# Performance work log

Measured on AMD Instinct MI355X. Metric: run time of the kernel, lower is better.

Reference implementation:

```python
import jax, jax.numpy as jnp
import numpy as np

EMBED, HEADS, WIN = 512, 1, 16  # head_dim == EMBED since HEADS == 1
B, S = 4, 2048


def setup_inputs() -> dict:
    key = jax.random.key(0)
    ks = jax.random.split(key, 9)
    sc = 1.0 / np.sqrt(EMBED)
    return {
        "x": jax.random.normal(ks[0], (B, S, EMBED), dtype=jnp.float32),
        "Wq": jax.random.normal(ks[1], (EMBED, EMBED), dtype=jnp.float32) * sc,
        "bq": jax.random.normal(ks[2], (EMBED,), dtype=jnp.float32) * 0.01,
        "Wk": jax.random.normal(ks[3], (EMBED, EMBED), dtype=jnp.float32) * sc,
        "bk": jax.random.normal(ks[4], (EMBED,), dtype=jnp.float32) * 0.01,
        "Wv": jax.random.normal(ks[5], (EMBED, EMBED), dtype=jnp.float32) * sc,
        "bv": jax.random.normal(ks[6], (EMBED,), dtype=jnp.float32) * 0.01,
        "Wo": jax.random.normal(ks[7], (EMBED, EMBED), dtype=jnp.float32) * sc,
        "bo": jax.random.normal(ks[8], (EMBED,), dtype=jnp.float32) * 0.01,
    }


def reference(x, Wq, bq, Wk, bk, Wv, bv, Wo, bo):
    Bsz, Sq, E = x.shape
    w = WIN
    W = 2 * w + 1  # window span
    # Pad sequence with zeros (as F.pad in the original); the Linear bias is
    # applied to padded positions too (linear(0) = bias), matching torch.
    xp = jnp.pad(x, ((0, 0), (w, w), (0, 0)))  # [B, S+2w, E]
    Qp = xp @ Wq.T + bq
    Kp = xp @ Wk.T + bk
    Vp = xp @ Wv.T + bv
    # Original energy: einsum('bswhd,bswhd->bswh') -> dot of Q and K at the
    # SAME window slot, so it collapses to a per-position scalar, then gathered.
    scale = 1.0 / float(E) ** 0.5  # head_dim == E since heads == 1
    e = jnp.sum(Qp * Kp, axis=-1) * scale  # [B, S+2w]
    idx = jnp.arange(Sq)[:, None] + jnp.arange(W)[None, :]  # [S, W] into padded
    ew = e[:, idx]  # [B, S, W]
    attn = jax.nn.softmax(ew, axis=2)  # softmax over window dim
    Vw = Vp[:, idx]  # [B, S, W, E]
    out = jnp.einsum('bsw,bswe->bse', attn, Vw)  # [B, S, E]
    return out @ Wo.T + bo
```

## Files before the change

kernel.cpp:

```cpp
#include <hip/hip_runtime.h>
#include <stdint.h>

#define SEQ 2048
#define BATCH 4
#define EMB 512
#define MTOT (BATCH * SEQ)
#define WIN 16
#define WINDOW 33

typedef uint32_t u32;
typedef unsigned short u16;
typedef __attribute__((ext_vector_type(8))) __bf16 bf16x8;
typedef __attribute__((ext_vector_type(4))) float f32x4;
typedef __attribute__((ext_vector_type(4))) u16 u16x4;
typedef __attribute__((ext_vector_type(8))) u16 u16x8;

__device__ __forceinline__ u16 f2bf(float f) {
  u32 u = __builtin_bit_cast(u32, f);
  u = (u + 0x7fffu + ((u >> 16) & 1u)) >> 16;
  return (u16)u;
}
__device__ __forceinline__ float bf2f(u16 v) {
  return __builtin_bit_cast(float, (u32)v << 16);
}
__device__ __forceinline__ void gload16(void* lds, const void* g) {
  __builtin_amdgcn_global_load_lds((const __attribute__((address_space(1))) u32*)g,
                                   (__attribute__((address_space(3))) u32*)lds, 16, 0, 0);
}
__device__ __forceinline__ void drain_stage() {
  asm volatile("s_waitcnt vmcnt(0) lgkmcnt(0)" ::: "memory");
}

__global__ void __launch_bounds__(256) prep3(
    const float* __restrict__ x, const float* __restrict__ Wq, const float* __restrict__ Wk,
    const float* __restrict__ Wv, const float* __restrict__ Wo,
    const float* __restrict__ bq, const float* __restrict__ bk,
    const float* __restrict__ bv, const float* __restrict__ bo,
    u16* __restrict__ xb, u16* __restrict__ Wqb, u16* __restrict__ Wkb,
    u16* __restrict__ Wob, u16* __restrict__ WvT,
    float* __restrict__ bc, float* __restrict__ econst) {
  __shared__ float sm[32][33];
  int b = blockIdx.x, t = threadIdx.x;
  if (b < 1024) {
    for (u32 i = b * 256 + t; i < (u32)(MTOT * EMB / 4); i += 1024 * 256) {
      float4 v = reinterpret_cast<const float4*>(x)[i];
      u16x4 o; o.x = f2bf(v.x); o.y = f2bf(v.y); o.z = f2bf(v.z); o.w = f2bf(v.w);
      reinterpret_cast<u16x4*>(xb)[i] = o;
    }
  } else if (b < 1792) {
    const float* S = (b < 1280) ? Wq : (b < 1536) ? Wk : Wo;
    u16* D = (b < 1280) ? Wqb : (b < 1536) ? Wkb : Wob;
    int cb = (b - 1024) & 255;
    int i = (cb * 256 + t) * 4;
    float4 v = *reinterpret_cast<const float4*>(S + i);
    u16x4 o; o.x = f2bf(v.x); o.y = f2bf(v.y); o.z = f2bf(v.z); o.w = f2bf(v.w);
    *reinterpret_cast<u16x4*>(D + i) = o;
  } else if (b < 2048) {
    int tb = b - 1792;
    int ti = tb >> 4, tj = tb & 15;
    int lr = t >> 5, lc = t & 31;
#pragma unroll
    for (int rr = 0; rr < 32; rr += 8)
      sm[rr + lr][lc] = Wv[(size_t)(ti * 32 + rr + lr) * EMB + tj * 32 + lc];
    __syncthreads();
    int jr = t >> 3, dc = (t & 7) * 4;
    u16x4 o;
#pragma unroll
    for (int c = 0; c < 4; ++c) o[c] = f2bf(sm[dc + c][jr]);
    *reinterpret_cast<u16x4*>(WvT + (size_t)(tj * 32 + jr) * EMB + ti * 32 + dc) = o;
  } else if (b < 2056) {
    float* sh = &sm[0][0];
    int cb = b - 2048;
    int ii = t >> 2, di = t & 3;
    int i = cb * 64 + ii;
    float s = 0.f;
    for (int d = di * 128; d < di * 128 + 128; ++d)
      s += Wo[(size_t)i * EMB + d] * bv[d];
    sh[t] = s;
    __syncthreads();
    if (di == 0) bc[i] = sh[t] + sh[t + 1] + sh[t + 2] + sh[t + 3] + bo[i];
  } else {
    float* sh = &sm[0][0];
    float s = bq[t] * bk[t] + bq[t + 256] * bk[t + 256];
    sh[t] = s;
    __syncthreads();
    for (int st = 128; st > 0; st >>= 1) {
      if (t < st) sh[t] += sh[t + st];
      __syncthreads();
    }
    if (t == 0) *econst = sh[0];
  }
}

__global__ void __launch_bounds__(256) gemm_qk(
    const u16* __restrict__ xb, const u16* __restrict__ Wqb, const u16* __restrict__ Wkb,
    const float* __restrict__ bq, const float* __restrict__ bk,
    float* __restrict__ e_part) {
  __shared__ u16 XL[64 * 64];
  __shared__ u16 QL[128 * 64];
  __shared__ u16 KL[128 * 64];
  int b = blockIdx.x;
  int wg = ((b & 7) << 6) + (b >> 3);
  int bx = wg >> 2, by = wg & 3;
  int t = threadIdx.x;
  int wave = t >> 6, lane = t & 63;
  int wr = wave >> 1, wc = wave & 1;
  int fr = lane & 15, fq = lane >> 4;
  int m0 = bx * 64, n0 = by * 128;
  f32x4 accQ[2][4] = {};
  f32x4 accK[2][4] = {};
  for (int kt = 0; kt < 8; ++kt) {
    __syncthreads();
    int kb = kt * 64;
#pragma unroll
    for (int it = 0; it < 2; ++it) {
      int chunk = t + it * 256;
      int row = chunk >> 3, col8 = (chunk & 7) * 8;
      gload16(XL + (size_t)(wave * 64 + it * 256) * 8, xb + (size_t)(m0 + row) * EMB + kb + col8);
    }
#pragma unroll
    for (int it = 0; it < 4; ++it) {
      int chunk = t + it * 256;
      int row = chunk >> 3, col8 = (chunk & 7) * 8;
      gload16(QL + (size_t)(wave * 64 + it * 256) * 8, Wqb + (size_t)(n0 + row) * EMB + kb + col8);
    }
#pragma unroll
    for (int it = 0; it < 4; ++it) {
      int chunk = t + it * 256;
      int row = chunk >> 3, col8 = (chunk & 7) * 8;
      gload16(KL + (size_t)(wave * 64 + it * 256) * 8, Wkb + (size_t)(n0 + row) * EMB + kb + col8);
    }
    drain_stage();
    __syncthreads();
    bf16x8 af[2][2];
#pragma unroll
    for (int m = 0; m < 2; ++m)
#pragma unroll
      for (int kk = 0; kk < 2; ++kk)
        af[m][kk] = *reinterpret_cast<const bf16x8*>(
            &XL[(wr * 32 + m * 16 + fr) * 64 + kk * 32 + fq * 8]);
#pragma unroll
    for (int kk = 0; kk < 2; ++kk)
#pragma unroll
      for (int n = 0; n < 4; ++n) {
        bf16x8 bq_ = *reinterpret_cast<const bf16x8*>(
            &QL[(wc * 64 + n * 16 + fr) * 64 + kk * 32 + fq * 8]);
#pragma unroll
        for (int m = 0; m < 2; ++m)
          accQ[m][n] = __builtin_amdgcn_mfma_f32_16x16x32_bf16(af[m][kk], bq_, accQ[m][n], 0, 0, 0);
        bf16x8 bk_ = *reinterpret_cast<const bf16x8*>(
            &KL[(wc * 64 + n * 16 + fr) * 64 + kk * 32 + fq * 8]);
#pragma unroll
        for (int m = 0; m < 2; ++m)
          accK[m][n] = __builtin_amdgcn_mfma_f32_16x16x32_bf16(af[m][kk], bk_, accK[m][n], 0, 0, 0);
      }
  }
  float bqv[4], bkv[4];
#pragma unroll
  for (int n = 0; n < 4; ++n) {
    int col = n0 + wc * 64 + n * 16 + fr;
    bqv[n] = bq[col];
    bkv[n] = bk[col];
  }
  int slot = by * 2 + wc;
#pragma unroll
  for (int m = 0; m < 2; ++m) {
#pragma unroll
    for (int r = 0; r < 4; ++r) {
      int row = m0 + wr * 32 + m * 16 + fq * 4 + r;
      float p = 0.f;
#pragma unroll
      for (int n = 0; n < 4; ++n)
        p += (accQ[m][n][r] + bqv[n]) * (accK[m][n][r] + bkv[n]);
      p += __shfl_xor(p, 1);
      p += __shfl_xor(p, 2);
      p += __shfl_xor(p, 4);
      p += __shfl_xor(p, 8);
      if (fr == 0) e_part[(size_t)slot * MTOT + row] = p;
    }
  }
}

__global__ void __launch_bounds__(256) window3(
    const u16* __restrict__ xb, const float* __restrict__ e_part,
    const float* __restrict__ econst_p, u16* __restrict__ y,
    const u16* __restrict__ Wob, const u16* __restrict__ WvT, u16* __restrict__ Wcb) {
  __shared__ __align__(16) char smem[51456];
  int b = blockIdx.x;
  int t = threadIdx.x;
  if (b >= 512) {
    u16* AL = (u16*)smem;
    u16* BL = (u16*)(smem + 4096);
    int wcb = b - 512;
    int i0 = (wcb >> 3) * 64, j0 = (wcb & 7) * 64;
    int wave = t >> 6, lane = t & 63;
    int wr = wave >> 1, wc = wave & 1;
    int fr = lane & 15, fq = lane >> 4;
    f32x4 acc[2][2] = {};
    for (int kt = 0; kt < 16; ++kt) {
      __syncthreads();
      int kb = kt * 32;
      int row = t >> 2, col8 = (t & 3) * 8;
      gload16(AL + (size_t)t * 8, Wob + (size_t)(i0 + row) * EMB + kb + col8);
      gload16(BL + (size_t)t * 8, WvT + (size_t)(j0 + row) * EMB + kb + col8);
      drain_stage();
      __syncthreads();
      bf16x8 af[2], bfv[2];
#pragma unroll
      for (int m = 0; m < 2; ++m)
        af[m] = *reinterpret_cast<const bf16x8*>(&AL[(wr * 32 + m * 16 + fr) * 32 + fq * 8]);
#pragma unroll
      for (int n = 0; n < 2; ++n)
        bfv[n] = *reinterpret_cast<const bf16x8*>(&BL[(wc * 32 + n * 16 + fr) * 32 + fq * 8]);
#pragma unroll
      for (int m = 0; m < 2; ++m)
#pragma unroll
        for (int n = 0; n < 2; ++n)
          acc[m][n] = __builtin_amdgcn_mfma_f32_16x16x32_bf16(af[m], bfv[n], acc[m][n], 0, 0, 0);
    }
#pragma unroll
    for (int m = 0; m < 2; ++m)
#pragma unroll
      for (int n = 0; n < 2; ++n)
#pragma unroll
        for (int r = 0; r < 4; ++r)
          Wcb[(size_t)(i0 + wr * 32 + m * 16 + fq * 4 + r) * EMB + j0 + wc * 32 + n * 16 + fr] =
              f2bf(acc[m][n][r]);
    return;
  }
  u16* Xt = (u16*)smem;
  float* eloc = (float*)(smem + 49152);
  float (*w)[WINDOW] = (float (*)[WINDOW])(smem + 49344);
  int swz = ((b & 7) << 6) + (b >> 3);
  int bb = swz >> 7;
  int s0 = (swz & 127) * 16;
  u16x8 stg[12];
#pragma unroll
  for (int i = 0; i < 12; ++i) {
    int chunk = t + i * 256;
    int row = chunk >> 6;
    int c8 = (chunk & 63) * 8;
    int n = s0 + row - WIN;
    if (n >= 0 && n < SEQ)
      stg[i] = *reinterpret_cast<const u16x8*>(xb + (size_t)(bb * SEQ + n) * EMB + c8);
    else
      stg[i] = (u16x8){0, 0, 0, 0, 0, 0, 0, 0};
  }
#pragma unroll
  for (int i = 0; i < 12; ++i) {
    int chunk = t + i * 256;
    int row = chunk >> 6;
    int c8 = (chunk & 63) * 8;
    *reinterpret_cast<u16x8*>(&Xt[(size_t)row * EMB + c8]) = stg[i];
  }
  const float scale = 0.044194173824159216f;
  float ec = *econst_p;
  if (t < 48) {
    int n = s0 + t - WIN;
    float raw = 0.f;
    if (n >= 0 && n < SEQ) {
      size_t idx = (size_t)bb * SEQ + n;
#pragma unroll
      for (int p = 0; p < 8; ++p) raw += e_part[(size_t)p * MTOT + idx];
    }
    eloc[t] = scale * (raw + ec);
  }
  __syncthreads();
  if (t < 16) {
    float ev[WINDOW];
    float mx = -1e30f;
#pragma unroll
    for (int j = 0; j < WINDOW; ++j) { ev[j] = eloc[t + j]; mx = fmaxf(mx, ev[j]); }
    float sum = 0.f;
#pragma unroll
    for (int j = 0; j < WINDOW; ++j) { float ex = __expf(ev[j] - mx); ev[j] = ex; sum += ex; }
    float inv = 1.f / sum;
#pragma unroll
    for (int j = 0; j < WINDOW; ++j) w[t][j] = ev[j] * inv;
  }
  __syncthreads();
  int cg = t & 63;
  int slg = t >> 6;
  int d0 = cg * 8;
  float oacc[4][8] = {};
  for (int ri = 0; ri < 36; ++ri) {
    int r = slg * 4 + ri;
    u16x8 v = *reinterpret_cast<const u16x8*>(&Xt[(size_t)r * EMB + d0]);
    float vf[8];
#pragma unroll
    for (int c = 0; c < 8; ++c) vf[c] = bf2f(v[c]);
#pragma unroll
    for (int q = 0; q < 4; ++q) {
      int j = ri - q;
      if (j >= 0 && j < WINDOW) {
        float wt = w[slg * 4 + q][j];
#pragma unroll
        for (int c = 0; c < 8; ++c) oacc[q][c] += wt * vf[c];
      }
    }
  }
#pragma unroll
  for (int q = 0; q < 4; ++q) {
    u16x8 o;
#pragma unroll
    for (int c = 0; c < 8; ++c) o[c] = f2bf(oacc[q][c]);
    *reinterpret_cast<u16x8*>(&y[(size_t)(bb * SEQ + s0 + slg * 4 + q) * EMB + d0]) = o;
  }
}

__global__ void __launch_bounds__(256) gemm_o(
    const u16* __restrict__ y, const u16* __restrict__ Wcb,
    const float* __restrict__ bc, float* __restrict__ out) {
  __shared__ u16 At2[64 * 32];
  __shared__ u16 Bt2[128 * 32];
  int b = blockIdx.x;
  int wg = ((b & 7) << 6) + (b >> 3);
  int bx = wg >> 2, by = wg & 3;
  int t = threadIdx.x;
  int wave = t >> 6, lane = t & 63;
  int wr = wave >> 1, wc = wave & 1;
  int fr = lane & 15, fq = lane >> 4;
  int m0 = bx * 64, n0 = by * 128;
  f32x4 acc[2][4] = {};
  for (int kt = 0; kt < EMB / 32; ++kt) {
    __syncthreads();
    int kb = kt * 32;
    {
      int row = t >> 2, col = (t & 3) * 8;
      gload16(At2 + (size_t)t * 8, y + (size_t)(m0 + row) * EMB + kb + col);
    }
#pragma unroll
    for (int it = 0; it < 2; ++it) {
      int chunk = t + it * 256;
      int row = chunk >> 2, col = (chunk & 3) * 8;
      gload16(Bt2 + (size_t)(wave * 64 + it * 256) * 8, Wcb + (size_t)(n0 + row) * EMB + kb + col);
    }
    drain_stage();
    __syncthreads();
    bf16x8 af[2], bfv[4];
#pragma unroll
    for (int m = 0; m < 2; ++m)
      af[m] = *reinterpret_cast<const bf16x8*>(&At2[(wr * 32 + m * 16 + fr) * 32 + fq * 8]);
#pragma unroll
    for (int n = 0; n < 4; ++n)
      bfv[n] = *reinterpret_cast<const bf16x8*>(&Bt2[(wc * 64 + n * 16 + fr) * 32 + fq * 8]);
#pragma unroll
    for (int m = 0; m < 2; ++m)
#pragma unroll
      for (int n = 0; n < 4; ++n)
        acc[m][n] = __builtin_amdgcn_mfma_f32_16x16x32_bf16(af[m], bfv[n], acc[m][n], 0, 0, 0);
  }
  float bcv[4];
#pragma unroll
  for (int n = 0; n < 4; ++n) bcv[n] = bc[n0 + wc * 64 + n * 16 + fr];
#pragma unroll
  for (int m = 0; m < 2; ++m)
#pragma unroll
    for (int n = 0; n < 4; ++n) {
      int col = n0 + wc * 64 + n * 16 + fr;
#pragma unroll
      for (int r = 0; r < 4; ++r) {
        int row = m0 + wr * 32 + m * 16 + fq * 4 + r;
        out[(size_t)row * EMB + col] = acc[m][n][r] + bcv[n];
      }
    }
}

extern "C" void kernel_launch(void* const* d_in, const int* in_sizes, int n_in,
                              void* d_out, int out_size, void* d_ws, size_t ws_size,
                              hipStream_t stream) {
  const float* x  = (const float*)d_in[0];
  const float* Wq = (const float*)d_in[1];
  const float* bq = (const float*)d_in[2];
  const float* Wk = (const float*)d_in[3];
  const float* bk = (const float*)d_in[4];
  const float* Wv = (const float*)d_in[5];
  const float* bv = (const float*)d_in[6];
  const float* Wo = (const float*)d_in[7];
  const float* bo = (const float*)d_in[8];
  float* out = (float*)d_out;

  char* ws = (char*)d_ws;
  u16* xb       = (u16*)(ws);
  u16* y        = (u16*)(ws + (8u << 20));
  u16* Wqb      = (u16*)(ws + (16u << 20));
  u16* Wkb      = (u16*)(ws + (16u << 20) + (512u << 10));
  u16* Wob      = (u16*)(ws + (16u << 20) + (1024u << 10));
  u16* WvT      = (u16*)(ws + (16u << 20) + (1536u << 10));
  u16* Wcb      = (u16*)(ws + (16u << 20) + (2048u << 10));
  float* e_part = (float*)(ws + (16u << 20) + (2560u << 10));
  float* bc     = (float*)(ws + (16u << 20) + (2816u << 10));
  float* econst = (float*)(ws + (16u << 20) + (2818u << 10));

  prep3<<<2057, 256, 0, stream>>>(x, Wq, Wk, Wv, Wo, bq, bk, bv, bo,
                                  xb, Wqb, Wkb, Wob, WvT, bc, econst);
  gemm_qk<<<512, 256, 0, stream>>>(xb, Wqb, Wkb, bq, bk, e_part);
  window3<<<576, 256, 0, stream>>>(xb, e_part, econst, y, Wob, WvT, Wcb);
  gemm_o<<<512, 256, 0, stream>>>(y, Wcb, bc, out);
}
```

Baseline: 59.48 us.

## Fuse x bf16 conversion into QK GEMM and shrink GEMM tiles

The separate pass that converted x to bf16 in the prep kernel is removed. The QK GEMM now loads fp32 x directly, converts it in registers, writes it to LDS, and has the by==0 column blocks also write the bf16 copy of x that the window kernel needs. Tiles shrink to 64x64 with a K-step of 32, so the grid grows to 1024 blocks and the number of partial e slots doubles to 16. This saves a full read and write of x, but each of the 8 column blocks now converts x from fp32 on its own, adding more VALU work and more fp32 global traffic into the GEMM, plus more partial sums to reduce.

```diff
diff --git a/kernel.cpp b/kernel.cpp
--- a/kernel.cpp
+++ b/kernel.cpp
@@ -31,32 +31,25 @@
   asm volatile("s_waitcnt vmcnt(0) lgkmcnt(0)" ::: "memory");
 }
 
-__global__ void __launch_bounds__(256) prep3(
-    const float* __restrict__ x, const float* __restrict__ Wq, const float* __restrict__ Wk,
+__global__ void __launch_bounds__(256) prep4(
+    const float* __restrict__ Wq, const float* __restrict__ Wk,
     const float* __restrict__ Wv, const float* __restrict__ Wo,
     const float* __restrict__ bq, const float* __restrict__ bk,
     const float* __restrict__ bv, const float* __restrict__ bo,
-    u16* __restrict__ xb, u16* __restrict__ Wqb, u16* __restrict__ Wkb,
-    u16* __restrict__ Wob, u16* __restrict__ WvT,
-    float* __restrict__ bc, float* __restrict__ econst) {
+    u16* __restrict__ Wqb, u16* __restrict__ Wkb, u16* __restrict__ Wob,
+    u16* __restrict__ WvT, float* __restrict__ bc, float* __restrict__ econst) {
   __shared__ float sm[32][33];
   int b = blockIdx.x, t = threadIdx.x;
-  if (b < 1024) {
-    for (u32 i = b * 256 + t; i < (u32)(MTOT * EMB / 4); i += 1024 * 256) {
-      float4 v = reinterpret_cast<const float4*>(x)[i];
-      u16x4 o; o.x = f2bf(v.x); o.y = f2bf(v.y); o.z = f2bf(v.z); o.w = f2bf(v.w);
-      reinterpret_cast<u16x4*>(xb)[i] = o;
-    }
-  } else if (b < 1792) {
-    const float* S = (b < 1280) ? Wq : (b < 1536) ? Wk : Wo;
-    u16* D = (b < 1280) ? Wqb : (b < 1536) ? Wkb : Wob;
-    int cb = (b - 1024) & 255;
+  if (b < 768) {
+    const float* S = (b < 256) ? Wq : (b < 512) ? Wk : Wo;
+    u16* D = (b < 256) ? Wqb : (b < 512) ? Wkb : Wob;
+    int cb = b & 255;
     int i = (cb * 256 + t) * 4;
     float4 v = *reinterpret_cast<const float4*>(S + i);
     u16x4 o; o.x = f2bf(v.x); o.y = f2bf(v.y); o.z = f2bf(v.z); o.w = f2bf(v.w);
     *reinterpret_cast<u16x4*>(D + i) = o;
-  } else if (b < 2048) {
-    int tb = b - 1792;
+  } else if (b < 1024) {
+    int tb = b - 768;
     int ti = tb >> 4, tj = tb & 15;
     int lr = t >> 5, lc = t & 31;
 #pragma unroll
@@ -68,9 +61,9 @@
 #pragma unroll
     for (int c = 0; c < 4; ++c) o[c] = f2bf(sm[dc + c][jr]);
     *reinterpret_cast<u16x4*>(WvT + (size_t)(tj * 32 + jr) * EMB + ti * 32 + dc) = o;
-  } else if (b < 2056) {
+  } else if (b < 1032) {
     float* sh = &sm[0][0];
-    int cb = b - 2048;
+    int cb = b - 1024;
     int ii = t >> 2, di = t & 3;
     int i = cb * 64 + ii;
     float s = 0.f;
@@ -92,73 +85,63 @@
   }
 }
 
-__global__ void __launch_bounds__(256) gemm_qk(
-    const u16* __restrict__ xb, const u16* __restrict__ Wqb, const u16* __restrict__ Wkb,
+__global__ void __launch_bounds__(256) gemm_qk2(
+    const float* __restrict__ x, const u16* __restrict__ Wqb, const u16* __restrict__ Wkb,
     const float* __restrict__ bq, const float* __restrict__ bk,
-    float* __restrict__ e_part) {
-  __shared__ u16 XL[64 * 64];
-  __shared__ u16 QL[128 * 64];
-  __shared__ u16 KL[128 * 64];
+    float* __restrict__ e_part, u16* __restrict__ xb) {
+  __shared__ u16 XL[64 * 32];
+  __shared__ u16 QL[64 * 32];
+  __shared__ u16 KL[64 * 32];
   int b = blockIdx.x;
-  int wg = ((b & 7) << 6) + (b >> 3);
-  int bx = wg >> 2, by = wg & 3;
+  int wg = ((b & 7) << 7) + (b >> 3);
+  int by = wg & 7, bx = wg >> 3;
   int t = threadIdx.x;
   int wave = t >> 6, lane = t & 63;
   int wr = wave >> 1, wc = wave & 1;
   int fr = lane & 15, fq = lane >> 4;
-  int m0 = bx * 64, n0 = by * 128;
-  f32x4 accQ[2][4] = {};
-  f32x4 accK[2][4] = {};
-  for (int kt = 0; kt < 8; ++kt) {
-    __syncthreads();
-    int kb = kt * 64;
-#pragma unroll
-    for (int it = 0; it < 2; ++it) {
-      int chunk = t + it * 256;
-      int row = chunk >> 3, col8 = (chunk & 7) * 8;
-      gload16(XL + (size_t)(wave * 64 + it * 256) * 8, xb + (size_t)(m0 + row) * EMB + kb + col8);
-    }
-#pragma unroll
-    for (int it = 0; it < 4; ++it) {
-      int chunk = t + it * 256;
-      int row = chunk >> 3, col8 = (chunk & 7) * 8;
-      gload16(QL + (size_t)(wave * 64 + it * 256) * 8, Wqb + (size_t)(n0 + row) * EMB + kb + col8);
-    }
-#pragma unroll
-    for (int it = 0; it < 4; ++it) {
-      int chunk = t + it * 256;
-      int row = chunk >> 3, col8 = (chunk & 7) * 8;
-      gload16(KL + (size_t)(wave * 64 + it * 256) * 8, Wkb + (size_t)(n0 + row) * EMB + kb + col8);
+  int m0 = bx * 64, n0 = by * 64;
+  bool emitX = (by == 0);
+  int srow = t >> 2, sc8 = (t & 3) * 8;
+  f32x4 accQ[2][2] = {};
+  f32x4 accK[2][2] = {};
+  for (int kt = 0; kt < 16; ++kt) {
+    __syncthreads();
+    int kb = kt * 32;
+    gload16(QL + (size_t)t * 8, Wqb + (size_t)(n0 + srow) * EMB + kb + sc8);
+    gload16(KL + (size_t)t * 8, Wkb + (size_t)(n0 + srow) * EMB + kb + sc8);
+    {
+      const float* xs = x + (size_t)(m0 + srow) * EMB + kb + sc8;
+      float4 v0 = *reinterpret_cast<const float4*>(xs);
+      float4 v1 = *reinterpret_cast<const float4*>(xs + 4);
+      u16x8 a8;
+      a8[0] = f2bf(v0.x); a8[1] = f2bf(v0.y); a8[2] = f2bf(v0.z); a8[3] = f2bf(v0.w);
+      a8[4] = f2bf(v1.x); a8[5] = f2bf(v1.y); a8[6] = f2bf(v1.z); a8[7] = f2bf(v1.w);
+      *reinterpret_cast<u16x8*>(&XL[srow * 32 + sc8]) = a8;
+      if (emitX)
+        *reinterpret_cast<u16x8*>(xb + (size_t)(m0 + srow) * EMB + kb + sc8) = a8;
     }
     drain_stage();
     __syncthreads();
-    bf16x8 af[2][2];
+    bf16x8 af[2];
 #pragma unroll
     for (int m = 0; m < 2; ++m)
-#pragma unroll
-      for (int kk = 0; kk < 2; ++kk)
-        af[m][kk] = *reinterpret_cast<const bf16x8*>(
-            &XL[(wr * 32 + m * 16 + fr) * 64 + kk * 32 + fq * 8]);
-#pragma unroll
-    for (int kk = 0; kk < 2; ++kk)
-#pragma unroll
-      for (int n = 0; n < 4; ++n) {
-        bf16x8 bq_ = *reinterpret_cast<const bf16x8*>(
-            &QL[(wc * 64 + n * 16 + fr) * 64 + kk * 32 + fq * 8]);
-#pragma unroll
-        for (int m = 0; m < 2; ++m)
-          accQ[m][n] = __builtin_amdgcn_mfma_f32_16x16x32_bf16(af[m][kk], bq_, accQ[m][n], 0, 0, 0);
-        bf16x8 bk_ = *reinterpret_cast<const bf16x8*>(
-            &KL[(wc * 64 + n * 16 + fr) * 64 + kk * 32 + fq * 8]);
-#pragma unroll
-        for (int m = 0; m < 2; ++m)
-          accK[m][n] = __builtin_amdgcn_mfma_f32_16x16x32_bf16(af[m][kk], bk_, accK[m][n], 0, 0, 0);
-      }
-  }
-  float bqv[4], bkv[4];
-#pragma unroll
-  for (int n = 0; n < 4; ++n) {
-    int col = n0 + wc * 64 + n * 16 + fr;
+      af[m] = *reinterpret_cast<const bf16x8*>(&XL[(wr * 32 + m * 16 + fr) * 32 + fq * 8]);
+#pragma unroll
+    for (int n = 0; n < 2; ++n) {
+      bf16x8 q8 = *reinterpret_cast<const bf16x8*>(&QL[(wc * 32 + n * 16 + fr) * 32 + fq * 8]);
+#pragma unroll
+      for (int m = 0; m < 2; ++m)
+        accQ[m][n] = __builtin_amdgcn_mfma_f32_16x16x32_bf16(af[m], q8, accQ[m][n], 0, 0, 0);
+      bf16x8 k8 = *reinterpret_cast<const bf16x8*>(&KL[(wc * 32 + n * 16 + fr) * 32 + fq * 8]);
+#pragma unroll
+      for (int m = 0; m < 2; ++m)
+        accK[m][n] = __builtin_amdgcn_mfma_f32_16x16x32_bf16(af[m], k8, accK[m][n], 0, 0, 0);
+    }
+  }
+  float bqv[2], bkv[2];
+#pragma unroll
+  for (int n = 0; n < 2; ++n) {
+    int col = n0 + wc * 32 + n * 16 + fr;
     bqv[n] = bq[col];
     bkv[n] = bk[col];
   }
@@ -170,7 +153,7 @@
       int row = m0 + wr * 32 + m * 16 + fq * 4 + r;
       float p = 0.f;
 #pragma unroll
-      for (int n = 0; n < 4; ++n)
+      for (int n = 0; n < 2; ++n)
         p += (accQ[m][n][r] + bqv[n]) * (accK[m][n][r] + bkv[n]);
       p += __shfl_xor(p, 1);
       p += __shfl_xor(p, 2);
@@ -261,7 +244,7 @@
     if (n >= 0 && n < SEQ) {
       size_t idx = (size_t)bb * SEQ + n;
 #pragma unroll
-      for (int p = 0; p < 8; ++p) raw += e_part[(size_t)p * MTOT + idx];
+      for (int p = 0; p < 16; ++p) raw += e_part[(size_t)p * MTOT + idx];
     }
     eloc[t] = scale * (raw + ec);
   }
@@ -389,12 +372,12 @@
   u16* WvT      = (u16*)(ws + (16u << 20) + (1536u << 10));
   u16* Wcb      = (u16*)(ws + (16u << 20) + (2048u << 10));
   float* e_part = (float*)(ws + (16u << 20) + (2560u << 10));
-  float* bc     = (float*)(ws + (16u << 20) + (2816u << 10));
-  float* econst = (float*)(ws + (16u << 20) + (2818u << 10));
-
-  prep3<<<2057, 256, 0, stream>>>(x, Wq, Wk, Wv, Wo, bq, bk, bv, bo,
-                                  xb, Wqb, Wkb, Wob, WvT, bc, econst);
-  gemm_qk<<<512, 256, 0, stream>>>(xb, Wqb, Wkb, bq, bk, e_part);
+  float* bc     = (float*)(ws + (16u << 20) + (3072u << 10));
+  float* econst = (float*)(ws + (16u << 20) + (3074u << 10));
+
+  prep4<<<1033, 256, 0, stream>>>(Wq, Wk, Wv, Wo, bq, bk, bv, bo,
+                                  Wqb, Wkb, Wob, WvT, bc, econst);
+  gemm_qk2<<<1024, 256, 0, stream>>>(x, Wqb, Wkb, bq, bk, e_part, xb);
   window3<<<576, 256, 0, stream>>>(xb, e_part, econst, y, Wob, WvT, Wcb);
   gemm_o<<<512, 256, 0, stream>>>(y, Wcb, bc, out);
 }
```

Measured after the change: 61.33 us. +3.1%, slower.

## Fold Wq^T Wk into one matrix so energy needs a single GEMM

Applied to the files above, without the earlier changes.

The per-position energy q·k is rewritten as x^T (Wq^T Wk) x + c·x + const. A 512x512 matrix A = Wk^T Wq is precomputed in a new small GEMM kernel, and the energy GEMM now multiplies x by A once instead of by both Wq and Wk. It then dots the result with fp32 x, which halves the MFMA work and the weight traffic. The Wo·WvT combine GEMM moves from the window kernel into the energy kernel. The cost is an extra kernel launch, extra transposes in prep, bf16 rounding of A, and uncoalesced fp32 reads of x in the epilogue.

```diff
diff --git a/kernel.cpp b/kernel.cpp
--- a/kernel.cpp
+++ b/kernel.cpp
@@ -31,46 +31,71 @@
   asm volatile("s_waitcnt vmcnt(0) lgkmcnt(0)" ::: "memory");
 }
 
-__global__ void __launch_bounds__(256) prep3(
+__global__ void __launch_bounds__(256) prep5(
     const float* __restrict__ x, const float* __restrict__ Wq, const float* __restrict__ Wk,
     const float* __restrict__ Wv, const float* __restrict__ Wo,
     const float* __restrict__ bq, const float* __restrict__ bk,
     const float* __restrict__ bv, const float* __restrict__ bo,
-    u16* __restrict__ xb, u16* __restrict__ Wqb, u16* __restrict__ Wkb,
+    u16* __restrict__ xb, u16* __restrict__ WqT, u16* __restrict__ WkT,
     u16* __restrict__ Wob, u16* __restrict__ WvT,
-    float* __restrict__ bc, float* __restrict__ econst) {
+    float* __restrict__ cvec, float* __restrict__ bc, float* __restrict__ econst) {
   __shared__ float sm[32][33];
   int b = blockIdx.x, t = threadIdx.x;
-  if (b < 1024) {
-    for (u32 i = b * 256 + t; i < (u32)(MTOT * EMB / 4); i += 1024 * 256) {
+  if (b < 512) {
+    for (u32 i = b * 256 + t; i < (u32)(MTOT * EMB / 4); i += 512 * 256) {
       float4 v = reinterpret_cast<const float4*>(x)[i];
       u16x4 o; o.x = f2bf(v.x); o.y = f2bf(v.y); o.z = f2bf(v.z); o.w = f2bf(v.w);
       reinterpret_cast<u16x4*>(xb)[i] = o;
     }
-  } else if (b < 1792) {
-    const float* S = (b < 1280) ? Wq : (b < 1536) ? Wk : Wo;
-    u16* D = (b < 1280) ? Wqb : (b < 1536) ? Wkb : Wob;
-    int cb = (b - 1024) & 255;
-    int i = (cb * 256 + t) * 4;
-    float4 v = *reinterpret_cast<const float4*>(S + i);
-    u16x4 o; o.x = f2bf(v.x); o.y = f2bf(v.y); o.z = f2bf(v.z); o.w = f2bf(v.w);
-    *reinterpret_cast<u16x4*>(D + i) = o;
-  } else if (b < 2048) {
-    int tb = b - 1792;
+  } else if (b < 1280 && !(b >= 1024 && b < 1280)) {
+    bool isQ = b < 768;
+    int tb = (b - 512) & 255;
+    const float* S = isQ ? Wq : Wk;
+    u16* D = isQ ? WqT : WkT;
     int ti = tb >> 4, tj = tb & 15;
     int lr = t >> 5, lc = t & 31;
 #pragma unroll
     for (int rr = 0; rr < 32; rr += 8)
-      sm[rr + lr][lc] = Wv[(size_t)(ti * 32 + rr + lr) * EMB + tj * 32 + lc];
+      sm[rr + lr][lc] = S[(size_t)(ti * 32 + rr + lr) * EMB + tj * 32 + lc];
     __syncthreads();
     int jr = t >> 3, dc = (t & 7) * 4;
     u16x4 o;
 #pragma unroll
     for (int c = 0; c < 4; ++c) o[c] = f2bf(sm[dc + c][jr]);
+    *reinterpret_cast<u16x4*>(D + (size_t)(tj * 32 + jr) * EMB + ti * 32 + dc) = o;
+  } else if (b < 1280) {
+    int cb = b - 1024;
+    int i = (cb * 256 + t) * 4;
+    float4 v = *reinterpret_cast<const float4*>(Wo + i);
+    u16x4 o; o.x = f2bf(v.x); o.y = f2bf(v.y); o.z = f2bf(v.z); o.w = f2bf(v.w);
+    *reinterpret_cast<u16x4*>(Wob + i) = o;
+  } else if (b < 1536) {
+    int tb = b - 1280;
+    int ti = tb >> 4, tj = tb & 15;
+    int lr = t >> 5, lc = t & 31;
+#pragma unroll
+    for (int rr = 0; rr < 32; rr += 8)
+      sm[rr + lr][lc] = Wv[(size_t)(ti * 32 + rr + lr) * EMB + tj * 32 + lc];
+    __syncthreads();
+    int jr = t >> 3, dc = (t & 7) * 4;
+    u16x4 o;
+#pragma unroll
+    for (int c = 0; c < 4; ++c) o[c] = f2bf(sm[dc + c][jr]);
     *reinterpret_cast<u16x4*>(WvT + (size_t)(tj * 32 + jr) * EMB + ti * 32 + dc) = o;
-  } else if (b < 2056) {
+  } else if (b < 1544) {
     float* sh = &sm[0][0];
-    int cb = b - 2048;
+    int cb = b - 1536;
+    int ii = t >> 2, di = t & 3;
+    int i = cb * 64 + ii;
+    float s = 0.f;
+    for (int d = di * 128; d < di * 128 + 128; ++d)
+      s += Wq[(size_t)d * EMB + i] * bk[d] + Wk[(size_t)d * EMB + i] * bq[d];
+    sh[t] = s;
+    __syncthreads();
+    if (di == 0) cvec[i] = sh[t] + sh[t + 1] + sh[t + 2] + sh[t + 3];
+  } else if (b < 1552) {
+    float* sh = &sm[0][0];
+    int cb = b - 1544;
     int ii = t >> 2, di = t & 3;
     int i = cb * 64 + ii;
     float s = 0.f;
@@ -92,76 +117,109 @@
   }
 }
 
-__global__ void __launch_bounds__(256) gemm_qk(
-    const u16* __restrict__ xb, const u16* __restrict__ Wqb, const u16* __restrict__ Wkb,
-    const float* __restrict__ bq, const float* __restrict__ bk,
-    float* __restrict__ e_part) {
-  __shared__ u16 XL[64 * 64];
-  __shared__ u16 QL[128 * 64];
-  __shared__ u16 KL[128 * 64];
+__device__ __forceinline__ void bt_tile64(
+    const u16* __restrict__ Arows, const u16* __restrict__ Brows, u16* __restrict__ C,
+    int i0, int j0, int t, char* smem) {
+  u16* AL = (u16*)smem;
+  u16* BL = (u16*)(smem + 4096);
+  int wave = t >> 6, lane = t & 63;
+  int wr = wave >> 1, wc = wave & 1;
+  int fr = lane & 15, fq = lane >> 4;
+  f32x4 acc[2][2] = {};
+  for (int kt = 0; kt < 16; ++kt) {
+    __syncthreads();
+    int kb = kt * 32;
+    int row = t >> 2, col8 = (t & 3) * 8;
+    gload16(AL + (size_t)t * 8, Arows + (size_t)(i0 + row) * EMB + kb + col8);
+    gload16(BL + (size_t)t * 8, Brows + (size_t)(j0 + row) * EMB + kb + col8);
+    drain_stage();
+    __syncthreads();
+    bf16x8 af[2], bfv[2];
+#pragma unroll
+    for (int m = 0; m < 2; ++m)
+      af[m] = *reinterpret_cast<const bf16x8*>(&AL[(wr * 32 + m * 16 + fr) * 32 + fq * 8]);
+#pragma unroll
+    for (int n = 0; n < 2; ++n)
+      bfv[n] = *reinterpret_cast<const bf16x8*>(&BL[(wc * 32 + n * 16 + fr) * 32 + fq * 8]);
+#pragma unroll
+    for (int m = 0; m < 2; ++m)
+#pragma unroll
+      for (int n = 0; n < 2; ++n)
+        acc[m][n] = __builtin_amdgcn_mfma_f32_16x16x32_bf16(af[m], bfv[n], acc[m][n], 0, 0, 0);
+  }
+#pragma unroll
+  for (int m = 0; m < 2; ++m) {
+    int wave2 = t >> 6;
+    int wr2 = wave2 >> 1, wc2 = wave2 & 1;
+    int fr2 = (t & 63) & 15, fq2 = (t & 63) >> 4;
+#pragma unroll
+    for (int n = 0; n < 2; ++n)
+#pragma unroll
+      for (int r = 0; r < 4; ++r)
+        C[(size_t)(i0 + wr2 * 32 + m * 16 + fq2 * 4 + r) * EMB + j0 + wc2 * 32 + n * 16 + fr2] =
+            f2bf(acc[m][n][r]);
+  }
+}
+
+__global__ void __launch_bounds__(256) gemm_atm(
+    const u16* __restrict__ WkT, const u16* __restrict__ WqT, u16* __restrict__ Atm) {
+  __shared__ __align__(16) char smem[8192];
   int b = blockIdx.x;
+  bt_tile64(WkT, WqT, Atm, (b >> 3) * 64, (b & 7) * 64, threadIdx.x, smem);
+}
+
+__global__ void __launch_bounds__(256) gemm_ewc(
+    const u16* __restrict__ xb, const u16* __restrict__ Atm,
+    const float* __restrict__ x, const float* __restrict__ cvec,
+    float* __restrict__ e_part,
+    const u16* __restrict__ Wob, const u16* __restrict__ WvT, u16* __restrict__ Wcb) {
+  __shared__ __align__(16) char smem[12288];
+  int b = blockIdx.x;
+  int t = threadIdx.x;
+  if (b >= 512) {
+    bt_tile64(Wob, WvT, Wcb, ((b - 512) >> 3) * 64, ((b - 512) & 7) * 64, t, smem);
+    return;
+  }
+  u16* At2 = (u16*)smem;
+  u16* Bt2 = (u16*)(smem + 4096);
   int wg = ((b & 7) << 6) + (b >> 3);
   int bx = wg >> 2, by = wg & 3;
-  int t = threadIdx.x;
   int wave = t >> 6, lane = t & 63;
   int wr = wave >> 1, wc = wave & 1;
   int fr = lane & 15, fq = lane >> 4;
   int m0 = bx * 64, n0 = by * 128;
-  f32x4 accQ[2][4] = {};
-  f32x4 accK[2][4] = {};
-  for (int kt = 0; kt < 8; ++kt) {
-    __syncthreads();
-    int kb = kt * 64;
+  f32x4 acc[2][4] = {};
+  for (int kt = 0; kt < EMB / 32; ++kt) {
+    __syncthreads();
+    int kb = kt * 32;
+    {
+      int row = t >> 2, col = (t & 3) * 8;
+      gload16(At2 + (size_t)t * 8, xb + (size_t)(m0 + row) * EMB + kb + col);
+    }
 #pragma unroll
     for (int it = 0; it < 2; ++it) {
       int chunk = t + it * 256;
-      int row = chunk >> 3, col8 = (chunk & 7) * 8;
-      gload16(XL + (size_t)(wave * 64 + it * 256) * 8, xb + (size_t)(m0 + row) * EMB + kb + col8);
-    }
-#pragma unroll
-    for (int it = 0; it < 4; ++it) {
-      int chunk = t + it * 256;
-      int row = chunk >> 3, col8 = (chunk & 7) * 8;
-      gload16(QL + (size_t)(wave * 64 + it * 256) * 8, Wqb + (size_t)(n0 + row) * EMB + kb + col8);
-    }
-#pragma unroll
-    for (int it = 0; it < 4; ++it) {
-      int chunk = t + it * 256;
-      int row = chunk >> 3, col8 = (chunk & 7) * 8;
-      gload16(KL + (size_t)(wave * 64 + it * 256) * 8, Wkb + (size_t)(n0 + row) * EMB + kb + col8);
+      int row = chunk >> 2, col = (chunk & 3) * 8;
+      gload16(Bt2 + (size_t)(wave * 64 + it * 256) * 8, Atm + (size_t)(n0 + row) * EMB + kb + col);
     }
     drain_stage();
     __syncthreads();
-    bf16x8 af[2][2];
-#pragma unroll
-    for (int m = 0; m < 2; ++m)
-#pragma unroll
-      for (int kk = 0; kk < 2; ++kk)
-        af[m][kk] = *reinterpret_cast<const bf16x8*>(
-            &XL[(wr * 32 + m * 16 + fr) * 64 + kk * 32 + fq * 8]);
-#pragma unroll
-    for (int kk = 0; kk < 2; ++kk)
-#pragma unroll
-      for (int n = 0; n < 4; ++n) {
-        bf16x8 bq_ = *reinterpret_cast<const bf16x8*>(
-            &QL[(wc * 64 + n * 16 + fr) * 64 + kk * 32 + fq * 8]);
-#pragma unroll
-        for (int m = 0; m < 2; ++m)
-          accQ[m][n] = __builtin_amdgcn_mfma_f32_16x16x32_bf16(af[m][kk], bq_, accQ[m][n], 0, 0, 0);
-        bf16x8 bk_ = *reinterpret_cast<const bf16x8*>(
-            &KL[(wc * 64 + n * 16 + fr) * 64 + kk * 32 + fq * 8]);
-#pragma unroll
-        for (int m = 0; m < 2; ++m)
-          accK[m][n] = __builtin_amdgcn_mfma_f32_16x16x32_bf16(af[m][kk], bk_, accK[m][n], 0, 0, 0);
-      }
-  }
-  float bqv[4], bkv[4];
-#pragma unroll
-  for (int n = 0; n < 4; ++n) {
-    int col = n0 + wc * 64 + n * 16 + fr;
-    bqv[n] = bq[col];
-    bkv[n] = bk[col];
-  }
+    bf16x8 af[2], bfv[4];
+#pragma unroll
+    for (int m = 0; m < 2; ++m)
+      af[m] = *reinterpret_cast<const bf16x8*>(&At2[(wr * 32 + m * 16 + fr) * 32 + fq * 8]);
+#pragma unroll
+    for (int n = 0; n < 4; ++n)
+      bfv[n] = *reinterpret_cast<const bf16x8*>(&Bt2[(wc * 64 + n * 16 + fr) * 32 + fq * 8]);
+#pragma unroll
+    for (int m = 0; m < 2; ++m)
+#pragma unroll
+      for (int n = 0; n < 4; ++n)
+        acc[m][n] = __builtin_amdgcn_mfma_f32_16x16x32_bf16(af[m], bfv[n], acc[m][n], 0, 0, 0);
+  }
+  float cv[4];
+#pragma unroll
+  for (int n = 0; n < 4; ++n) cv[n] = cvec[n0 + wc * 64 + n * 16 + fr];
   int slot = by * 2 + wc;
 #pragma unroll
   for (int m = 0; m < 2; ++m) {
@@ -170,8 +228,10 @@
       int row = m0 + wr * 32 + m * 16 + fq * 4 + r;
       float p = 0.f;
 #pragma unroll
-      for (int n = 0; n < 4; ++n)
-        p += (accQ[m][n][r] + bqv[n]) * (accK[m][n][r] + bkv[n]);
+      for (int n = 0; n < 4; ++n) {
+        int col = n0 + wc * 64 + n * 16 + fr;
+        p += (acc[m][n][r] + cv[n]) * x[(size_t)row * EMB + col];
+      }
       p += __shfl_xor(p, 1);
       p += __shfl_xor(p, 2);
       p += __shfl_xor(p, 4);
@@ -181,59 +241,17 @@
   }
 }
 
-__global__ void __launch_bounds__(256) window3(
+__global__ void __launch_bounds__(256) window4(
     const u16* __restrict__ xb, const float* __restrict__ e_part,
-    const float* __restrict__ econst_p, u16* __restrict__ y,
-    const u16* __restrict__ Wob, const u16* __restrict__ WvT, u16* __restrict__ Wcb) {
-  __shared__ __align__(16) char smem[51456];
+    const float* __restrict__ econst_p, u16* __restrict__ y) {
+  __shared__ u16 Xt[48 * EMB];
+  __shared__ float eloc[48];
+  __shared__ float w[16][WINDOW];
   int b = blockIdx.x;
-  int t = threadIdx.x;
-  if (b >= 512) {
-    u16* AL = (u16*)smem;
-    u16* BL = (u16*)(smem + 4096);
-    int wcb = b - 512;
-    int i0 = (wcb >> 3) * 64, j0 = (wcb & 7) * 64;
-    int wave = t >> 6, lane = t & 63;
-    int wr = wave >> 1, wc = wave & 1;
-    int fr = lane & 15, fq = lane >> 4;
-    f32x4 acc[2][2] = {};
-    for (int kt = 0; kt < 16; ++kt) {
-      __syncthreads();
-      int kb = kt * 32;
-      int row = t >> 2, col8 = (t & 3) * 8;
-      gload16(AL + (size_t)t * 8, Wob + (size_t)(i0 + row) * EMB + kb + col8);
-      gload16(BL + (size_t)t * 8, WvT + (size_t)(j0 + row) * EMB + kb + col8);
-      drain_stage();
-      __syncthreads();
-      bf16x8 af[2], bfv[2];
-#pragma unroll
-      for (int m = 0; m < 2; ++m)
-        af[m] = *reinterpret_cast<const bf16x8*>(&AL[(wr * 32 + m * 16 + fr) * 32 + fq * 8]);
-#pragma unroll
-      for (int n = 0; n < 2; ++n)
-        bfv[n] = *reinterpret_cast<const bf16x8*>(&BL[(wc * 32 + n * 16 + fr) * 32 + fq * 8]);
-#pragma unroll
-      for (int m = 0; m < 2; ++m)
-#pragma unroll
-        for (int n = 0; n < 2; ++n)
-          acc[m][n] = __builtin_amdgcn_mfma_f32_16x16x32_bf16(af[m], bfv[n], acc[m][n], 0, 0, 0);
-    }
-#pragma unroll
-    for (int m = 0; m < 2; ++m)
-#pragma unroll
-      for (int n = 0; n < 2; ++n)
-#pragma unroll
-        for (int r = 0; r < 4; ++r)
-          Wcb[(size_t)(i0 + wr * 32 + m * 16 + fq * 4 + r) * EMB + j0 + wc * 32 + n * 16 + fr] =
-              f2bf(acc[m][n][r]);
-    return;
-  }
-  u16* Xt = (u16*)smem;
-  float* eloc = (float*)(smem + 49152);
-  float (*w)[WINDOW] = (float (*)[WINDOW])(smem + 49344);
   int swz = ((b & 7) << 6) + (b >> 3);
   int bb = swz >> 7;
   int s0 = (swz & 127) * 16;
+  int t = threadIdx.x;
   u16x8 stg[12];
 #pragma unroll
   for (int i = 0; i < 12; ++i) {
@@ -383,18 +401,21 @@
   char* ws = (char*)d_ws;
   u16* xb       = (u16*)(ws);
   u16* y        = (u16*)(ws + (8u << 20));
-  u16* Wqb      = (u16*)(ws + (16u << 20));
-  u16* Wkb      = (u16*)(ws + (16u << 20) + (512u << 10));
+  u16* WqT      = (u16*)(ws + (16u << 20));
+  u16* WkT      = (u16*)(ws + (16u << 20) + (512u << 10));
   u16* Wob      = (u16*)(ws + (16u << 20) + (1024u << 10));
   u16* WvT      = (u16*)(ws + (16u << 20) + (1536u << 10));
-  u16* Wcb      = (u16*)(ws + (16u << 20) + (2048u << 10));
-  float* e_part = (float*)(ws + (16u << 20) + (2560u << 10));
-  float* bc     = (float*)(ws + (16u << 20) + (2816u << 10));
-  float* econst = (float*)(ws + (16u << 20) + (2818u << 10));
-
-  prep3<<<2057, 256, 0, stream>>>(x, Wq, Wk, Wv, Wo, bq, bk, bv, bo,
-                                  xb, Wqb, Wkb, Wob, WvT, bc, econst);
-  gemm_qk<<<512, 256, 0, stream>>>(xb, Wqb, Wkb, bq, bk, e_part);
-  window3<<<576, 256, 0, stream>>>(xb, e_part, econst, y, Wob, WvT, Wcb);
+  u16* Atm      = (u16*)(ws + (16u << 20) + (2048u << 10));
+  u16* Wcb      = (u16*)(ws + (16u << 20) + (2560u << 10));
+  float* e_part = (float*)(ws + (16u << 20) + (3072u << 10));
+  float* cvec   = (float*)(ws + (16u << 20) + (3328u << 10));
+  float* bc     = (float*)(ws + (16u << 20) + (3330u << 10));
+  float* econst = (float*)(ws + (16u << 20) + (3332u << 10));
+
+  prep5<<<1553, 256, 0, stream>>>(x, Wq, Wk, Wv, Wo, bq, bk, bv, bo,
+                                  xb, WqT, WkT, Wob, WvT, cvec, bc, econst);
+  gemm_atm<<<64, 256, 0, stream>>>(WkT, WqT, Atm);
+  gemm_ewc<<<576, 256, 0, stream>>>(xb, Atm, x, cvec, e_part, Wob, WvT, Wcb);
+  window4<<<512, 256, 0, stream>>>(xb, e_part, econst, y);
   gemm_o<<<512, 256, 0, stream>>>(y, Wcb, bc, out);
 }
```

New measurement: 68.28 us. +14.8%, slower.
